# Optimization experiments

Measured on AMD Instinct MI355X. Metric: run time of the kernel, lower is better.

The kernel has to match this reference:

```python
import jax, jax.numpy as jnp
import numpy as np

S_N = 100000   # number of students (embedding rows)
K_N = 30       # knowledge dim; must equal stu_dim=30 per the torch code
N_OUT = 1024   # number of exercises / output dim
B = 4096       # batch size
K_SEL = 3      # k_n_select
NVARS = 2 ** K_SEL - 2  # 6


def setup_inputs() -> dict:
    key = jax.random.key(0)
    ks = jax.random.split(key, 12)
    stu_id = jax.random.randint(ks[0], (B,), 0, S_N)
    exer_id = jax.random.randint(ks[1], (B,), 0, N_OUT)  # unused by forward, kept for fidelity
    kn_emb = jax.random.normal(ks[2], (B, K_N), jnp.float32)  # unused by forward
    # q matrix: exactly 3 ones per row -> sorted column indices (matches boolean-mask gather order)
    rng = np.random.default_rng(0)
    q_idx = np.stack([np.sort(rng.choice(K_N, K_SEL, replace=False)) for _ in range(N_OUT)])
    q_idx = jnp.asarray(q_idx, dtype=jnp.int32)  # [N_OUT, 3]
    emb = jax.random.normal(ks[3], (S_N, 30), jnp.float32) * 0.05
    fm_vars = jnp.abs(jax.random.normal(ks[4], (NVARS, N_OUT), jnp.float32)) * 0.1 + (1.0 / K_SEL)
    def lin(k, fan_out, fan_in):
        std = (2.0 / (fan_in + fan_out)) ** 0.5  # xavier normal
        return jax.random.normal(k, (fan_out, fan_in), jnp.float32) * std
    w1 = lin(ks[5], 256, N_OUT); b1 = jnp.zeros((256,), jnp.float32)
    w2 = lin(ks[6], 128, 256);   b2 = jnp.zeros((128,), jnp.float32)
    w3 = lin(ks[7], N_OUT, 128); b3 = jnp.zeros((N_OUT,), jnp.float32)
    return {"stu_id": stu_id, "exer_id": exer_id, "kn_emb": kn_emb, "q_idx": q_idx,
            "emb": emb, "fm_vars": fm_vars,
            "w1": w1, "b1": b1, "w2": w2, "b2": b2, "w3": w3, "b3": b3}


def _chi_fm(fm_vars):
    # fuzzy-measure construction for k_n_select=3 (subset lattice hardcoded, matches torch loop)
    chi = jnp.abs(fm_vars)            # [6, N_OUT]
    f0, f1 = chi[0], chi[1]
    f2 = jnp.maximum(f0, f1) + chi[2]
    f3 = chi[3]
    f4 = jnp.maximum(f3, f0) + chi[4]
    f5 = jnp.maximum(f3, f1) + chi[5]
    FM = jnp.stack([f0, f1, f2, f3, f4, f5, jnp.ones_like(f0)], axis=0)  # [7, N_OUT]
    return jnp.minimum(FM, 1.0).T     # [N_OUT, 7]


def reference(stu_id, exer_id, kn_emb, q_idx, emb, fm_vars, w1, b1, w2, b2, w3, b3):
    stu = jnp.take(emb, stu_id, axis=0)          # [B, 30]
    sel = jax.nn.sigmoid(stu)                     # [B, K_N]
    inputs = sel[:, q_idx]                        # gather -> [B, N_OUT, 3]
    idx = jnp.argsort(-inputs, axis=2)            # descending sort indices
    sv = jnp.take_along_axis(inputs, idx, axis=2) # sorted values, descending
    # diff with trailing zero: sv[k] - sv[k+1]
    diffs = sv - jnp.concatenate([sv[:, :, 1:], jnp.zeros_like(sv[:, :, :1])], axis=2)
    out_idx = jnp.cumsum(2 ** idx, axis=2) - 1    # subset node index in [0, 6], distinct per row
    bI = jnp.arange(inputs.shape[0])[:, None, None]
    nI = jnp.arange(inputs.shape[1])[None, :, None]
    alpha = jnp.zeros(inputs.shape[:2] + (NVARS + 1,), sv.dtype).at[bI, nI, out_idx].set(diffs)
    FM = _chi_fm(fm_vars)                          # [N_OUT, 7]
    C = jnp.sum(alpha * FM[None], axis=2)          # Choquet integral [B, N_OUT]
    h = jax.nn.relu(C @ w1.T + b1)                 # dropout is identity in eval
    h = jax.nn.relu(h @ w2.T + b2)
    return jax.nn.sigmoid(h @ w3.T + b3)           # [B, N_OUT]
```

## Files before the change

### kernel.cpp

```cpp
#include <hip/hip_runtime.h>
#include <math.h>

#define K_N   30
#define N_OUT 1024
#define BB    4096
#define SMEM_BYTES 155648

typedef unsigned short ushort_t;
typedef __attribute__((ext_vector_type(8))) short bf16x8;
typedef __attribute__((ext_vector_type(4))) float f32x4;

#define GLOBAL_AS(p) ((const __attribute__((address_space(1))) void*)(p))
#define LDS_AS(p)    ((__attribute__((address_space(3))) void*)(p))

#define MFMA(a, b, c) (c) = __builtin_amdgcn_mfma_f32_16x16x32_bf16((a), (b), (c), 0, 0, 0)
#define MF3(ah, al, bh, bl, c) do { MFMA(ah, bh, c); MFMA(ah, bl, c); MFMA(al, bh, c); } while (0)

__device__ __forceinline__ ushort_t f2bf(float x) {
  union { float f; unsigned u; } a; a.f = x;
  unsigned r = a.u + 0x7FFFu + ((a.u >> 16) & 1u);
  return (ushort_t)(r >> 16);
}
__device__ __forceinline__ float bf2f(ushort_t h) {
  union { float f; unsigned u; } a; a.u = ((unsigned)h) << 16;
  return a.f;
}

__device__ __forceinline__ float choquet_one(float v0, float v1, float v2,
                                             float F0, float F1, float F2,
                                             float F3, float F4, float F5) {
  bool c01 = v1 > v0, c02 = v2 > v0, c12 = v2 > v1;
  int r0 = (int)c01 + (int)c02;
  int r1 = (int)(!c01) + (int)c12;
  int p0 = (r0 == 0) ? 0 : ((r1 == 0) ? 1 : 2);
  int p1 = (r0 == 1) ? 0 : ((r1 == 1) ? 1 : 2);
  int p2 = 3 - p0 - p1;
  float sv0 = (p0 == 0) ? v0 : ((p0 == 1) ? v1 : v2);
  float sv1 = (p1 == 0) ? v0 : ((p1 == 1) ? v1 : v2);
  float sv2 = (p2 == 0) ? v0 : ((p2 == 1) ? v1 : v2);
  float fm0 = (p0 == 0) ? F0 : ((p0 == 1) ? F1 : F3);
  float fm1 = (p2 == 2) ? F2 : ((p2 == 1) ? F4 : F5);
  return (sv0 - sv1) * fm0 + (sv1 - sv2) * fm1 + sv2;
}

__global__ __launch_bounds__(512) void cicdm_split(
    const float* __restrict__ w1, const float* __restrict__ w2,
    const float* __restrict__ w3, ushort_t* __restrict__ w1h,
    ushort_t* __restrict__ w1l, ushort_t* __restrict__ w2h,
    ushort_t* __restrict__ w2l, ushort_t* __restrict__ w3h,
    ushort_t* __restrict__ w3l) {
  int i = blockIdx.x * 512 + threadIdx.x;
  float v;
  ushort_t *ph, *pl;
  int off;
  if (i < 262144) {
    off = i; v = w1[off]; ph = w1h; pl = w1l;
  } else if (i < 294912) {
    off = i - 262144; v = w2[off]; ph = w2h; pl = w2l;
  } else {
    off = i - 294912; v = w3[off]; ph = w3h; pl = w3l;
  }
  ushort_t h = f2bf(v);
  ph[off] = h;
  pl[off] = f2bf(v - bf2f(h));
}

__global__ __launch_bounds__(512, 2) void cicdm_fused(
    const int* __restrict__ stu_id, const int* __restrict__ q_idx,
    const float* __restrict__ emb, const float* __restrict__ fm_vars,
    const float* __restrict__ b1, const float* __restrict__ b2,
    const float* __restrict__ b3, const ushort_t* __restrict__ w1h,
    const ushort_t* __restrict__ w1l, const ushort_t* __restrict__ w2h,
    const ushort_t* __restrict__ w2l, const ushort_t* __restrict__ w3h,
    const ushort_t* __restrict__ w3l, float* __restrict__ out) {
  extern __shared__ __align__(16) char dsm[];
  ushort_t* sC = (ushort_t*)dsm;
  ushort_t* wq = (ushort_t*)(dsm + 65536 + (threadIdx.x >> 6) * 8192);
  float* sSel = (float*)(dsm + 65536);
  ushort_t* sH1 = (ushort_t*)(dsm + 131072);
  ushort_t* sH2 = (ushort_t*)(dsm + 147456);

  const int bid = blockIdx.x, tid = threadIdx.x;
  const int lane = tid & 63, wid = tid >> 6;
  const int lrow = lane & 15, lc = lane >> 4;
  const int row0 = bid * 16;

  if (tid < 16 * K_N) {
    int r = tid / K_N, c = tid % K_N;
    float x = emb[(size_t)stu_id[row0 + r] * K_N + c];
    sSel[r * 32 + c] = 1.f / (1.f + expf(-x));
  }
  __syncthreads();
  {
    const int n0 = tid * 2;
    const int qa0 = q_idx[n0 * 3 + 0], qa1 = q_idx[n0 * 3 + 1],
              qa2 = q_idx[n0 * 3 + 2];
    const int qb0 = q_idx[n0 * 3 + 3], qb1 = q_idx[n0 * 3 + 4],
              qb2 = q_idx[n0 * 3 + 5];
    float fa[6], fb[6];
#pragma unroll
    for (int v = 0; v < 6; ++v) {
      fa[v] = fabsf(fm_vars[v * N_OUT + n0]);
      fb[v] = fabsf(fm_vars[v * N_OUT + n0 + 1]);
    }
    float A0 = fminf(fa[0], 1.f), A1 = fminf(fa[1], 1.f), A3 = fminf(fa[3], 1.f);
    float A2 = fminf(fmaxf(fa[0], fa[1]) + fa[2], 1.f);
    float A4 = fminf(fmaxf(fa[3], fa[0]) + fa[4], 1.f);
    float A5 = fminf(fmaxf(fa[3], fa[1]) + fa[5], 1.f);
    float B0 = fminf(fb[0], 1.f), B1 = fminf(fb[1], 1.f), B3 = fminf(fb[3], 1.f);
    float B2 = fminf(fmaxf(fb[0], fb[1]) + fb[2], 1.f);
    float B4 = fminf(fmaxf(fb[3], fb[0]) + fb[4], 1.f);
    float B5 = fminf(fmaxf(fb[3], fb[1]) + fb[5], 1.f);
    const int kc = n0 >> 3, wi = n0 & 7;
#pragma unroll 4
    for (int r = 0; r < 16; ++r) {
      const float* sr = sSel + r * 32;
      float cA = choquet_one(sr[qa0], sr[qa1], sr[qa2], A0, A1, A2, A3, A4, A5);
      float cB = choquet_one(sr[qb0], sr[qb1], sr[qb2], B0, B1, B2, B3, B4, B5);
      ushort_t hA = f2bf(cA), hB = f2bf(cB);
      ushort_t lA = f2bf(cA - bf2f(hA)), lB = f2bf(cB - bf2f(hB));
      int byo = r * 2048 + ((kc ^ (r & 7)) * 8 + wi) * 2;
      *(unsigned*)((char*)sC + byo) = (unsigned)hA | ((unsigned)hB << 16);
      *(unsigned*)((char*)sC + 32768 + byo) = (unsigned)lA | ((unsigned)lB << 16);
    }
  }
  __syncthreads();

  {
    auto stage = [&](int cur, int kc) {
#pragma unroll
      for (int j = 0; j < 2; ++j) {
        int col = wid * 32 + j * 16 + lrow;
        const ushort_t* s0 = w1h + (size_t)col * 1024 + kc * 32 + lc * 8;
        const ushort_t* s1 = w1l + (size_t)col * 1024 + kc * 32 + lc * 8;
        __builtin_amdgcn_global_load_lds(GLOBAL_AS(s0),
            LDS_AS(wq + cur * 2048 + j * 1024), 16, 0, 0);
        __builtin_amdgcn_global_load_lds(GLOBAL_AS(s1),
            LDS_AS(wq + cur * 2048 + j * 1024 + 512), 16, 0, 0);
      }
    };
    f32x4 acc0 = {}, acc1 = {};
    stage(0, 0);
#pragma unroll 2
    for (int kc = 0; kc < 32; ++kc) {
      int cur = kc & 1;
      if (kc < 31) {
        stage(cur ^ 1, kc + 1);
        asm volatile("s_waitcnt vmcnt(4)" ::: "memory");
      } else {
        asm volatile("s_waitcnt vmcnt(0)" ::: "memory");
      }
      int pA = (kc * 4 + lc) ^ (lrow & 7);
      bf16x8 ah = *(const bf16x8*)(sC + lrow * 1024 + pA * 8);
      bf16x8 al = *(const bf16x8*)(sC + 16384 + lrow * 1024 + pA * 8);
      bf16x8 b0h = *(const bf16x8*)(wq + cur * 2048 + lane * 8);
      bf16x8 b0l = *(const bf16x8*)(wq + cur * 2048 + 512 + lane * 8);
      bf16x8 b1h = *(const bf16x8*)(wq + cur * 2048 + 1024 + lane * 8);
      bf16x8 b1l = *(const bf16x8*)(wq + cur * 2048 + 1536 + lane * 8);
      MF3(ah, al, b0h, b0l, acc0);
      MF3(ah, al, b1h, b1l, acc1);
    }
#pragma unroll
    for (int j = 0; j < 2; ++j) {
      f32x4 a = j ? acc1 : acc0;
      int col = wid * 32 + j * 16 + lrow;
      float bv = b1[col];
      int kc = col >> 3, wi = col & 7;
#pragma unroll
      for (int rr = 0; rr < 4; ++rr) {
        int r = lc * 4 + rr;
        float v = fmaxf(a[rr] + bv, 0.f);
        ushort_t h = f2bf(v);
        int byo = r * 512 + ((kc ^ (r & 7)) * 8 + wi) * 2;
        *(ushort_t*)((char*)sH1 + byo) = h;
        *(ushort_t*)((char*)sH1 + 8192 + byo) = f2bf(v - bf2f(h));
      }
    }
  }
  __syncthreads();

  {
    auto stage = [&](int cur, int ks) {
      int col = wid * 16 + lrow;
      const ushort_t* s0 = w2h + (size_t)col * 256 + ks * 32 + lc * 8;
      const ushort_t* s1 = w2l + (size_t)col * 256 + ks * 32 + lc * 8;
      __builtin_amdgcn_global_load_lds(GLOBAL_AS(s0), LDS_AS(wq + cur * 2048),
                                       16, 0, 0);
      __builtin_amdgcn_global_load_lds(GLOBAL_AS(s1),
                                       LDS_AS(wq + cur * 2048 + 512), 16, 0, 0);
    };
    f32x4 acc = {};
    stage(0, 0);
#pragma unroll 2
    for (int ks = 0; ks < 8; ++ks) {
      int cur = ks & 1;
      if (ks < 7) {
        stage(cur ^ 1, ks + 1);
        asm volatile("s_waitcnt vmcnt(2)" ::: "memory");
      } else {
        asm volatile("s_waitcnt vmcnt(0)" ::: "memory");
      }
      int pA = (ks * 4 + lc) ^ (lrow & 7);
      bf16x8 ah = *(const bf16x8*)(sH1 + lrow * 256 + pA * 8);
      bf16x8 al = *(const bf16x8*)(sH1 + 4096 + lrow * 256 + pA * 8);
      bf16x8 bh = *(const bf16x8*)(wq + cur * 2048 + lane * 8);
      bf16x8 bl = *(const bf16x8*)(wq + cur * 2048 + 512 + lane * 8);
      MF3(ah, al, bh, bl, acc);
    }
    int col = wid * 16 + lrow;
    float bv = b2[col];
    int kc = col >> 3, wi = col & 7;
#pragma unroll
    for (int rr = 0; rr < 4; ++rr) {
      int r = lc * 4 + rr;
      float v = fmaxf(acc[rr] + bv, 0.f);
      ushort_t h = f2bf(v);
      int byo = r * 256 + ((kc ^ (r & 7)) * 8 + wi) * 2;
      *(ushort_t*)((char*)sH2 + byo) = h;
      *(ushort_t*)((char*)sH2 + 4096 + byo) = f2bf(v - bf2f(h));
    }
  }
  __syncthreads();

  {
    auto stage = [&](int cur, int u) {
      int ks = u >> 2, cp = u & 3;
#pragma unroll
      for (int j = 0; j < 2; ++j) {
        int col = wid * 128 + cp * 32 + j * 16 + lrow;
        const ushort_t* s0 = w3h + (size_t)col * 128 + ks * 32 + lc * 8;
        const ushort_t* s1 = w3l + (size_t)col * 128 + ks * 32 + lc * 8;
        __builtin_amdgcn_global_load_lds(GLOBAL_AS(s0),
            LDS_AS(wq + cur * 2048 + j * 1024), 16, 0, 0);
        __builtin_amdgcn_global_load_lds(GLOBAL_AS(s1),
            LDS_AS(wq + cur * 2048 + j * 1024 + 512), 16, 0, 0);
      }
    };
    f32x4 acc[8] = {};
    bf16x8 ah = {}, al = {};
    stage(0, 0);
#pragma unroll
    for (int u = 0; u < 16; ++u) {
      int cur = u & 1, ks = u >> 2, cp = u & 3;
      if (u < 15) {
        stage(cur ^ 1, u + 1);
        asm volatile("s_waitcnt vmcnt(4)" ::: "memory");
      } else {
        asm volatile("s_waitcnt vmcnt(0)" ::: "memory");
      }
      if (cp == 0) {
        int pA = (ks * 4 + lc) ^ (lrow & 7);
        ah = *(const bf16x8*)(sH2 + lrow * 128 + pA * 8);
        al = *(const bf16x8*)(sH2 + 2048 + lrow * 128 + pA * 8);
      }
      bf16x8 b0h = *(const bf16x8*)(wq + cur * 2048 + lane * 8);
      bf16x8 b0l = *(const bf16x8*)(wq + cur * 2048 + 512 + lane * 8);
      bf16x8 b1h = *(const bf16x8*)(wq + cur * 2048 + 1024 + lane * 8);
      bf16x8 b1l = *(const bf16x8*)(wq + cur * 2048 + 1536 + lane * 8);
      MF3(ah, al, b0h, b0l, acc[cp * 2 + 0]);
      MF3(ah, al, b1h, b1l, acc[cp * 2 + 1]);
    }
#pragma unroll
    for (int cp = 0; cp < 4; ++cp)
#pragma unroll
      for (int j = 0; j < 2; ++j) {
        int col = wid * 128 + cp * 32 + j * 16 + lrow;
        float bv = b3[col];
#pragma unroll
        for (int rr = 0; rr < 4; ++rr) {
          int row = row0 + lc * 4 + rr;
          float v = acc[cp * 2 + j][rr] + bv;
          out[(size_t)row * N_OUT + col] = 1.f / (1.f + expf(-v));
        }
      }
  }
}

extern "C" void kernel_launch(void* const* d_in, const int* in_sizes, int n_in,
                              void* d_out, int out_size, void* d_ws,
                              size_t ws_size, hipStream_t stream) {
  const int* stu_id = (const int*)d_in[0];
  const int* q_idx = (const int*)d_in[3];
  const float* emb = (const float*)d_in[4];
  const float* fm_vars = (const float*)d_in[5];
  const float* w1 = (const float*)d_in[6];
  const float* b1 = (const float*)d_in[7];
  const float* w2 = (const float*)d_in[8];
  const float* b2 = (const float*)d_in[9];
  const float* w3 = (const float*)d_in[10];
  const float* b3 = (const float*)d_in[11];
  float* out = (float*)d_out;

  char* ws = (char*)d_ws;
  size_t off = 0;
  auto alloc = [&](size_t bytes) {
    void* p = ws + off;
    off += (bytes + 255) & ~(size_t)255;
    return p;
  };
  ushort_t* w1h = (ushort_t*)alloc(256 * N_OUT * 2);
  ushort_t* w1l = (ushort_t*)alloc(256 * N_OUT * 2);
  ushort_t* w2h = (ushort_t*)alloc(128 * 256 * 2);
  ushort_t* w2l = (ushort_t*)alloc(128 * 256 * 2);
  ushort_t* w3h = (ushort_t*)alloc(N_OUT * 128 * 2);
  ushort_t* w3l = (ushort_t*)alloc(N_OUT * 128 * 2);

  (void)hipFuncSetAttribute((const void*)cicdm_fused,
                            hipFuncAttributeMaxDynamicSharedMemorySize,
                            SMEM_BYTES);

  cicdm_split<<<832, 512, 0, stream>>>(w1, w2, w3, w1h, w1l, w2h, w2l, w3h,
                                       w3l);
  cicdm_fused<<<256, 512, SMEM_BYTES, stream>>>(stu_id, q_idx, emb, fm_vars,
                                                b1, b2, b3, w1h, w1l, w2h, w2l,
                                                w3h, w3l, out);
}
```

Baseline: 144.5 us.

## Pre-swizzle weights into MFMA fragment layout and load directly to registers

The split kernel now writes the bf16 hi/lo weight copies in a fragment-major layout matching the MFMA B-operand, so each lane reads one contiguous 16-byte vector. The fused kernel drops the global-to-LDS staging buffers and waitcnt pipeline, instead prefetching weight fragments straight into registers four steps ahead. It also splits accumulators into two chains so the three MFMAs per step carry fewer back-to-back dependencies, and shrinks shared memory to 80KB by aliasing H1/H2 over earlier buffers. Register pressure rises and latency hiding now depends on the compiler's scheduling of the register prefetch.

Measured after the change: 120.0 us. -16.9%, faster.

```diff
diff --git a/kernel.cpp b/kernel.cpp
--- a/kernel.cpp
+++ b/kernel.cpp
@@ -4,17 +4,13 @@
 #define K_N   30
 #define N_OUT 1024
 #define BB    4096
-#define SMEM_BYTES 155648
+#define SMEM_BYTES 81920
 
 typedef unsigned short ushort_t;
 typedef __attribute__((ext_vector_type(8))) short bf16x8;
 typedef __attribute__((ext_vector_type(4))) float f32x4;
 
-#define GLOBAL_AS(p) ((const __attribute__((address_space(1))) void*)(p))
-#define LDS_AS(p)    ((__attribute__((address_space(3))) void*)(p))
-
 #define MFMA(a, b, c) (c) = __builtin_amdgcn_mfma_f32_16x16x32_bf16((a), (b), (c), 0, 0, 0)
-#define MF3(ah, al, bh, bl, c) do { MFMA(ah, bh, c); MFMA(ah, bl, c); MFMA(al, bh, c); } while (0)
 
 __device__ __forceinline__ ushort_t f2bf(float x) {
   union { float f; unsigned u; } a; a.f = x;
@@ -45,40 +41,50 @@
 
 __global__ __launch_bounds__(512) void cicdm_split(
     const float* __restrict__ w1, const float* __restrict__ w2,
-    const float* __restrict__ w3, ushort_t* __restrict__ w1h,
-    ushort_t* __restrict__ w1l, ushort_t* __restrict__ w2h,
-    ushort_t* __restrict__ w2l, ushort_t* __restrict__ w3h,
-    ushort_t* __restrict__ w3l) {
+    const float* __restrict__ w3, ushort_t* __restrict__ w1fh,
+    ushort_t* __restrict__ w1fl, ushort_t* __restrict__ w2fh,
+    ushort_t* __restrict__ w2fl, ushort_t* __restrict__ w3fh,
+    ushort_t* __restrict__ w3fl) {
   int i = blockIdx.x * 512 + threadIdx.x;
   float v;
   ushort_t *ph, *pl;
-  int off;
+  int dst;
   if (i < 262144) {
-    off = i; v = w1[off]; ph = w1h; pl = w1l;
+    int c = i >> 10, k = i & 1023;
+    v = w1[i];
+    dst = ((c >> 4) * 32 + (k >> 5)) * 512 + (((k >> 3) & 3) * 16 + (c & 15)) * 8 + (k & 7);
+    ph = w1fh; pl = w1fl;
   } else if (i < 294912) {
-    off = i - 262144; v = w2[off]; ph = w2h; pl = w2l;
+    int i2 = i - 262144;
+    int c = i2 >> 8, k = i2 & 255;
+    v = w2[i2];
+    dst = ((c >> 4) * 8 + (k >> 5)) * 512 + (((k >> 3) & 3) * 16 + (c & 15)) * 8 + (k & 7);
+    ph = w2fh; pl = w2fl;
   } else {
-    off = i - 294912; v = w3[off]; ph = w3h; pl = w3l;
+    int i3 = i - 294912;
+    int c = i3 >> 7, k = i3 & 127;
+    v = w3[i3];
+    dst = ((c >> 4) * 4 + (k >> 5)) * 512 + (((k >> 3) & 3) * 16 + (c & 15)) * 8 + (k & 7);
+    ph = w3fh; pl = w3fl;
   }
   ushort_t h = f2bf(v);
-  ph[off] = h;
-  pl[off] = f2bf(v - bf2f(h));
+  ph[dst] = h;
+  pl[dst] = f2bf(v - bf2f(h));
 }
 
 __global__ __launch_bounds__(512, 2) void cicdm_fused(
     const int* __restrict__ stu_id, const int* __restrict__ q_idx,
     const float* __restrict__ emb, const float* __restrict__ fm_vars,
     const float* __restrict__ b1, const float* __restrict__ b2,
-    const float* __restrict__ b3, const ushort_t* __restrict__ w1h,
-    const ushort_t* __restrict__ w1l, const ushort_t* __restrict__ w2h,
-    const ushort_t* __restrict__ w2l, const ushort_t* __restrict__ w3h,
-    const ushort_t* __restrict__ w3l, float* __restrict__ out) {
+    const float* __restrict__ b3, const ushort_t* __restrict__ w1fh,
+    const ushort_t* __restrict__ w1fl, const ushort_t* __restrict__ w2fh,
+    const ushort_t* __restrict__ w2fl, const ushort_t* __restrict__ w3fh,
+    const ushort_t* __restrict__ w3fl, float* __restrict__ out) {
   extern __shared__ __align__(16) char dsm[];
   ushort_t* sC = (ushort_t*)dsm;
-  ushort_t* wq = (ushort_t*)(dsm + 65536 + (threadIdx.x >> 6) * 8192);
   float* sSel = (float*)(dsm + 65536);
-  ushort_t* sH1 = (ushort_t*)(dsm + 131072);
-  ushort_t* sH2 = (ushort_t*)(dsm + 147456);
+  ushort_t* sH1 = (ushort_t*)(dsm + 65536);
+  ushort_t* sH2 = (ushort_t*)dsm;
 
   const int bid = blockIdx.x, tid = threadIdx.x;
   const int lane = tid & 63, wid = tid >> 6;
@@ -127,51 +133,47 @@
   __syncthreads();
 
   {
-    auto stage = [&](int cur, int kc) {
-#pragma unroll
-      for (int j = 0; j < 2; ++j) {
-        int col = wid * 32 + j * 16 + lrow;
-        const ushort_t* s0 = w1h + (size_t)col * 1024 + kc * 32 + lc * 8;
-        const ushort_t* s1 = w1l + (size_t)col * 1024 + kc * 32 + lc * 8;
-        __builtin_amdgcn_global_load_lds(GLOBAL_AS(s0),
-            LDS_AS(wq + cur * 2048 + j * 1024), 16, 0, 0);
-        __builtin_amdgcn_global_load_lds(GLOBAL_AS(s1),
-            LDS_AS(wq + cur * 2048 + j * 1024 + 512), 16, 0, 0);
-      }
-    };
-    f32x4 acc0 = {}, acc1 = {};
-    stage(0, 0);
-#pragma unroll 2
-    for (int kc = 0; kc < 32; ++kc) {
-      int cur = kc & 1;
-      if (kc < 31) {
-        stage(cur ^ 1, kc + 1);
-        asm volatile("s_waitcnt vmcnt(4)" ::: "memory");
+    const ushort_t* baseH = w1fh + wid * 32768 + lane * 8;
+    const ushort_t* baseL = w1fl + wid * 32768 + lane * 8;
+    bf16x8 ph[4], pl[4];
+    f32x4 cA1 = {}, cA2 = {}, cB1 = {}, cB2 = {};
+    bf16x8 ah = {}, al = {};
+#define LD1(s, d)                                                   \
+  do {                                                              \
+    int o = (((s) & 1) * 16384) + (((s) >> 1) * 512);               \
+    ph[d] = *(const bf16x8*)(baseH + o);                            \
+    pl[d] = *(const bf16x8*)(baseL + o);                            \
+  } while (0)
+    LD1(0, 0); LD1(1, 1); LD1(2, 2); LD1(3, 3);
+#pragma unroll
+    for (int s = 0; s < 64; ++s) {
+      int kc = s >> 1;
+      if ((s & 1) == 0) {
+        int pA = (kc * 4 + lc) ^ (lrow & 7);
+        ah = *(const bf16x8*)(sC + lrow * 1024 + pA * 8);
+        al = *(const bf16x8*)(sC + 16384 + lrow * 1024 + pA * 8);
+      }
+      bf16x8 wh = ph[s & 3], wl = pl[s & 3];
+      if ((s & 1) == 0) {
+        MFMA(ah, wh, cA1); MFMA(ah, wl, cA2); MFMA(al, wh, cA2);
       } else {
-        asm volatile("s_waitcnt vmcnt(0)" ::: "memory");
-      }
-      int pA = (kc * 4 + lc) ^ (lrow & 7);
-      bf16x8 ah = *(const bf16x8*)(sC + lrow * 1024 + pA * 8);
-      bf16x8 al = *(const bf16x8*)(sC + 16384 + lrow * 1024 + pA * 8);
-      bf16x8 b0h = *(const bf16x8*)(wq + cur * 2048 + lane * 8);
-      bf16x8 b0l = *(const bf16x8*)(wq + cur * 2048 + 512 + lane * 8);
-      bf16x8 b1h = *(const bf16x8*)(wq + cur * 2048 + 1024 + lane * 8);
-      bf16x8 b1l = *(const bf16x8*)(wq + cur * 2048 + 1536 + lane * 8);
-      MF3(ah, al, b0h, b0l, acc0);
-      MF3(ah, al, b1h, b1l, acc1);
-    }
+        MFMA(ah, wh, cB1); MFMA(ah, wl, cB2); MFMA(al, wh, cB2);
+      }
+      if (s + 4 < 64) LD1(s + 4, s & 3);
+    }
+#undef LD1
+    f32x4 accs[2] = {cA1 + cA2, cB1 + cB2};
 #pragma unroll
     for (int j = 0; j < 2; ++j) {
-      f32x4 a = j ? acc1 : acc0;
       int col = wid * 32 + j * 16 + lrow;
       float bv = b1[col];
-      int kc = col >> 3, wi = col & 7;
+      int kc2 = col >> 3, wi2 = col & 7;
 #pragma unroll
       for (int rr = 0; rr < 4; ++rr) {
         int r = lc * 4 + rr;
-        float v = fmaxf(a[rr] + bv, 0.f);
+        float v = fmaxf(accs[j][rr] + bv, 0.f);
         ushort_t h = f2bf(v);
-        int byo = r * 512 + ((kc ^ (r & 7)) * 8 + wi) * 2;
+        int byo = r * 512 + ((kc2 ^ (r & 7)) * 8 + wi2) * 2;
         *(ushort_t*)((char*)sH1 + byo) = h;
         *(ushort_t*)((char*)sH1 + 8192 + byo) = f2bf(v - bf2f(h));
       }
@@ -180,42 +182,37 @@
   __syncthreads();
 
   {
-    auto stage = [&](int cur, int ks) {
-      int col = wid * 16 + lrow;
-      const ushort_t* s0 = w2h + (size_t)col * 256 + ks * 32 + lc * 8;
-      const ushort_t* s1 = w2l + (size_t)col * 256 + ks * 32 + lc * 8;
-      __builtin_amdgcn_global_load_lds(GLOBAL_AS(s0), LDS_AS(wq + cur * 2048),
-                                       16, 0, 0);
-      __builtin_amdgcn_global_load_lds(GLOBAL_AS(s1),
-                                       LDS_AS(wq + cur * 2048 + 512), 16, 0, 0);
-    };
-    f32x4 acc = {};
-    stage(0, 0);
-#pragma unroll 2
-    for (int ks = 0; ks < 8; ++ks) {
-      int cur = ks & 1;
-      if (ks < 7) {
-        stage(cur ^ 1, ks + 1);
-        asm volatile("s_waitcnt vmcnt(2)" ::: "memory");
-      } else {
-        asm volatile("s_waitcnt vmcnt(0)" ::: "memory");
-      }
-      int pA = (ks * 4 + lc) ^ (lrow & 7);
+    const ushort_t* baseH = w2fh + wid * 4096 + lane * 8;
+    const ushort_t* baseL = w2fl + wid * 4096 + lane * 8;
+    bf16x8 ph[4], pl[4];
+    f32x4 c1 = {}, c2 = {};
+#define LD2(s, d)                                                   \
+  do {                                                              \
+    int o = (s) * 512;                                              \
+    ph[d] = *(const bf16x8*)(baseH + o);                            \
+    pl[d] = *(const bf16x8*)(baseL + o);                            \
+  } while (0)
+    LD2(0, 0); LD2(1, 1); LD2(2, 2); LD2(3, 3);
+#pragma unroll
+    for (int s = 0; s < 8; ++s) {
+      int pA = (s * 4 + lc) ^ (lrow & 7);
       bf16x8 ah = *(const bf16x8*)(sH1 + lrow * 256 + pA * 8);
       bf16x8 al = *(const bf16x8*)(sH1 + 4096 + lrow * 256 + pA * 8);
-      bf16x8 bh = *(const bf16x8*)(wq + cur * 2048 + lane * 8);
-      bf16x8 bl = *(const bf16x8*)(wq + cur * 2048 + 512 + lane * 8);
-      MF3(ah, al, bh, bl, acc);
-    }
+      bf16x8 wh = ph[s & 3], wl = pl[s & 3];
+      MFMA(ah, wh, c1); MFMA(ah, wl, c2); MFMA(al, wh, c2);
+      if (s + 4 < 8) LD2(s + 4, s & 3);
+    }
+#undef LD2
+    f32x4 acc = c1 + c2;
     int col = wid * 16 + lrow;
     float bv = b2[col];
-    int kc = col >> 3, wi = col & 7;
+    int kc2 = col >> 3, wi2 = col & 7;
 #pragma unroll
     for (int rr = 0; rr < 4; ++rr) {
       int r = lc * 4 + rr;
       float v = fmaxf(acc[rr] + bv, 0.f);
       ushort_t h = f2bf(v);
-      int byo = r * 256 + ((kc ^ (r & 7)) * 8 + wi) * 2;
+      int byo = r * 256 + ((kc2 ^ (r & 7)) * 8 + wi2) * 2;
       *(ushort_t*)((char*)sH2 + byo) = h;
       *(ushort_t*)((char*)sH2 + 4096 + byo) = f2bf(v - bf2f(h));
     }
@@ -223,56 +220,43 @@
   __syncthreads();
 
   {
-    auto stage = [&](int cur, int u) {
-      int ks = u >> 2, cp = u & 3;
-#pragma unroll
-      for (int j = 0; j < 2; ++j) {
-        int col = wid * 128 + cp * 32 + j * 16 + lrow;
-        const ushort_t* s0 = w3h + (size_t)col * 128 + ks * 32 + lc * 8;
-        const ushort_t* s1 = w3l + (size_t)col * 128 + ks * 32 + lc * 8;
-        __builtin_amdgcn_global_load_lds(GLOBAL_AS(s0),
-            LDS_AS(wq + cur * 2048 + j * 1024), 16, 0, 0);
-        __builtin_amdgcn_global_load_lds(GLOBAL_AS(s1),
-            LDS_AS(wq + cur * 2048 + j * 1024 + 512), 16, 0, 0);
-      }
-    };
-    f32x4 acc[8] = {};
+    const ushort_t* baseH = w3fh + wid * 16384 + lane * 8;
+    const ushort_t* baseL = w3fl + wid * 16384 + lane * 8;
+    bf16x8 ph[4], pl[4];
+    f32x4 a1[8] = {}, a2[8] = {};
     bf16x8 ah = {}, al = {};
-    stage(0, 0);
-#pragma unroll
-    for (int u = 0; u < 16; ++u) {
-      int cur = u & 1, ks = u >> 2, cp = u & 3;
-      if (u < 15) {
-        stage(cur ^ 1, u + 1);
-        asm volatile("s_waitcnt vmcnt(4)" ::: "memory");
-      } else {
-        asm volatile("s_waitcnt vmcnt(0)" ::: "memory");
-      }
-      if (cp == 0) {
+#define LD3(s, d)                                                   \
+  do {                                                              \
+    int o = (((s) & 7) * 2048) + (((s) >> 3) * 512);                \
+    ph[d] = *(const bf16x8*)(baseH + o);                            \
+    pl[d] = *(const bf16x8*)(baseL + o);                            \
+  } while (0)
+    LD3(0, 0); LD3(1, 1); LD3(2, 2); LD3(3, 3);
+#pragma unroll
+    for (int s = 0; s < 32; ++s) {
+      int ks = s >> 3, cg = s & 7;
+      if (cg == 0) {
         int pA = (ks * 4 + lc) ^ (lrow & 7);
         ah = *(const bf16x8*)(sH2 + lrow * 128 + pA * 8);
         al = *(const bf16x8*)(sH2 + 2048 + lrow * 128 + pA * 8);
       }
-      bf16x8 b0h = *(const bf16x8*)(wq + cur * 2048 + lane * 8);
-      bf16x8 b0l = *(const bf16x8*)(wq + cur * 2048 + 512 + lane * 8);
-      bf16x8 b1h = *(const bf16x8*)(wq + cur * 2048 + 1024 + lane * 8);
-      bf16x8 b1l = *(const bf16x8*)(wq + cur * 2048 + 1536 + lane * 8);
-      MF3(ah, al, b0h, b0l, acc[cp * 2 + 0]);
-      MF3(ah, al, b1h, b1l, acc[cp * 2 + 1]);
-    }
-#pragma unroll
-    for (int cp = 0; cp < 4; ++cp)
-#pragma unroll
-      for (int j = 0; j < 2; ++j) {
-        int col = wid * 128 + cp * 32 + j * 16 + lrow;
-        float bv = b3[col];
-#pragma unroll
-        for (int rr = 0; rr < 4; ++rr) {
-          int row = row0 + lc * 4 + rr;
-          float v = acc[cp * 2 + j][rr] + bv;
-          out[(size_t)row * N_OUT + col] = 1.f / (1.f + expf(-v));
-        }
-      }
+      bf16x8 wh = ph[s & 3], wl = pl[s & 3];
+      MFMA(ah, wh, a1[cg]); MFMA(ah, wl, a2[cg]); MFMA(al, wh, a2[cg]);
+      if (s + 4 < 32) LD3(s + 4, s & 3);
+    }
+#undef LD3
+#pragma unroll
+    for (int cg = 0; cg < 8; ++cg) {
+      f32x4 acc = a1[cg] + a2[cg];
+      int col = wid * 128 + cg * 16 + lrow;
+      float bv = b3[col];
+#pragma unroll
+      for (int rr = 0; rr < 4; ++rr) {
+        int row = row0 + lc * 4 + rr;
+        float v = acc[rr] + bv;
+        out[(size_t)row * N_OUT + col] = 1.f / (1.f + expf(-v));
+      }
+    }
   }
 }
 
@@ -298,20 +282,20 @@
     off += (bytes + 255) & ~(size_t)255;
     return p;
   };
-  ushort_t* w1h = (ushort_t*)alloc(256 * N_OUT * 2);
-  ushort_t* w1l = (ushort_t*)alloc(256 * N_OUT * 2);
-  ushort_t* w2h = (ushort_t*)alloc(128 * 256 * 2);
-  ushort_t* w2l = (ushort_t*)alloc(128 * 256 * 2);
-  ushort_t* w3h = (ushort_t*)alloc(N_OUT * 128 * 2);
-  ushort_t* w3l = (ushort_t*)alloc(N_OUT * 128 * 2);
+  ushort_t* w1fh = (ushort_t*)alloc(256 * N_OUT * 2);
+  ushort_t* w1fl = (ushort_t*)alloc(256 * N_OUT * 2);
+  ushort_t* w2fh = (ushort_t*)alloc(128 * 256 * 2);
+  ushort_t* w2fl = (ushort_t*)alloc(128 * 256 * 2);
+  ushort_t* w3fh = (ushort_t*)alloc(N_OUT * 128 * 2);
+  ushort_t* w3fl = (ushort_t*)alloc(N_OUT * 128 * 2);
 
   (void)hipFuncSetAttribute((const void*)cicdm_fused,
                             hipFuncAttributeMaxDynamicSharedMemorySize,
                             SMEM_BYTES);
 
-  cicdm_split<<<832, 512, 0, stream>>>(w1, w2, w3, w1h, w1l, w2h, w2l, w3h,
-                                       w3l);
+  cicdm_split<<<832, 512, 0, stream>>>(w1, w2, w3, w1fh, w1fl, w2fh, w2fl,
+                                       w3fh, w3fl);
   cicdm_fused<<<256, 512, SMEM_BYTES, stream>>>(stu_id, q_idx, emb, fm_vars,
-                                                b1, b2, b3, w1h, w1l, w2h, w2l,
-                                                w3h, w3l, out);
-}
+                                                b1, b2, b3, w1fh, w1fl, w2fh,
+                                                w2fl, w3fh, w3fl, out);
+}
```
